# Kernel optimization log

Hardware: AMD Instinct MI355X
Metric: run time of the kernel (lower is better)

## Reference

```python
import jax, jax.numpy as jnp
import numpy as np

N = 50000      # nodes per type
E = 262144     # edges per relation
D_IN = 256; D_OUT = 256; D_ATT = 64
NEG_SLOPE = 0.2


def setup_inputs() -> dict:
    key = jax.random.key(0)
    ks = jax.random.split(key, 22)
    rn = lambda k, s, sc=0.05: jax.random.normal(k, s, jnp.float32) * sc
    ri = lambda k, s: jax.random.randint(k, s, 0, N, jnp.int32)
    return {
        "hA": jax.random.normal(ks[0], (N, D_IN), jnp.float32),
        "hB": jax.random.normal(ks[1], (N, D_IN), jnp.float32),
        "Wself": rn(ks[2], (2, D_IN, D_OUT)),
        "bself": rn(ks[3], (2, D_OUT), 0.01),
        "Wq": rn(ks[4], (2, D_OUT, D_ATT)),
        "bq": rn(ks[5], (2, D_ATT), 0.01),
        "Wk": rn(ks[6], (2, D_OUT, D_ATT)),
        "bk": rn(ks[7], (2, D_ATT), 0.01),
        "Wal": rn(ks[8], (2, D_ATT)),
        "bal": rn(ks[9], (2,), 0.01),
        "War": rn(ks[10], (2, D_ATT)),
        "bar": rn(ks[11], (2,), 0.01),
        "Wsrc": rn(ks[12], (2, D_IN, D_OUT)),
        "bsrc": rn(ks[13], (2, D_OUT), 0.01),
        "Wdst": rn(ks[14], (2, D_IN, D_OUT)),
        "bdst": rn(ks[15], (2, D_OUT), 0.01),
        "attn_v": rn(ks[16], (2, D_OUT)),
        "gbias": rn(ks[17], (2, D_OUT), 0.01),
        "eab_src": ri(ks[18], (E,)),
        "eab_dst": ri(ks[19], (E,)),
        "eba_src": ri(ks[20], (E,)),
        "eba_dst": ri(ks[21], (E,)),
    }


def _gatv2(h_src, h_dst, src, dst, Ws, bs, Wd, bd, av, gb, n_dst):
    """DGL GATv2Conv, num_heads=1: e_uv = av . leaky_relu(fc_src(h)[u] + fc_dst(h)[v]),
    edge-softmax over incoming edges per dst, message = alpha * fc_src(h)[u], + bias."""
    ft_s = h_src @ Ws + bs                              # (Ns, D)
    ft_d = h_dst @ Wd + bd                              # (Nd, D)
    e = jax.nn.leaky_relu(ft_s[src] + ft_d[dst], NEG_SLOPE)  # (E, D)
    logits = e @ av                                     # (E,)
    m = jax.ops.segment_max(logits, dst, num_segments=n_dst)
    m = jnp.where(jnp.isfinite(m), m, 0.0)              # zero-in-degree safety
    ex = jnp.exp(logits - m[dst])
    den = jax.ops.segment_sum(ex, dst, num_segments=n_dst)
    alpha = ex / jnp.where(den[dst] > 0, den[dst], 1.0)  # (E,) edge softmax
    out = jax.ops.segment_sum(alpha[:, None] * ft_s[src], dst, num_segments=n_dst) + gb
    return out, alpha


def _forward(hA, hB, Wself, bself, Wq, bq, Wk, bk, Wal, bal, War, bar,
             Wsrc, bsrc, Wdst, bdst, attn_v, gbias,
             eab_src, eab_dst, eba_src, eba_dst):
    h = [hA, hB]
    z = [h[t] @ Wself[t] + bself[t] for t in range(2)]       # HeteroLinear W_self
    q = [z[t] @ Wq[t] + bq[t] for t in range(2)]
    k = [z[t] @ Wk[t] + bk[t] for t in range(2)]
    h_l = [k[t] @ Wal[t] + bal[t] for t in range(2)]          # (N,) = W_al(key)
    h_r = [q[t] @ War[t] + bar[t] for t in range(2)]          # (N,) = W_ar(query)
    att_self = [jax.nn.elu(h_l[t] + h_r[t]) for t in range(2)]

    # relation "ab": A -> B (etype index 0)
    rst_ab, a_ab = _gatv2(hA, hB, eab_src, eab_dst,
                          Wsrc[0], bsrc[0], Wdst[0], bdst[0], attn_v[0], gbias[0], N)
    eatt_b = jax.nn.elu((rst_ab @ Wk[1] + bk[1]) @ Wal[1] + bal[1] + h_r[1])
    # relation "ba": B -> A (etype index 1)
    rst_ba, a_ba = _gatv2(hB, hA, eba_src, eba_dst,
                          Wsrc[1], bsrc[1], Wdst[1], bdst[1], attn_v[1], gbias[1], N)
    eatt_a = jax.nn.elu((rst_ba @ Wk[0] + bk[0]) @ Wal[0] + bal[0] + h_r[0])

    attA = jax.nn.softmax(jnp.stack([att_self[0], eatt_a]), axis=0)  # (2, N)
    attB = jax.nn.softmax(jnp.stack([att_self[1], eatt_b]), axis=0)
    rstA = jax.nn.elu(attA[0][:, None] * z[0] + attA[1][:, None] * rst_ba)
    rstB = jax.nn.elu(attB[0][:, None] * z[1] + attB[1][:, None] * rst_ab)
    return jnp.stack([rstA, rstB])  # (2, N, D_OUT)


def reference(hA, hB, Wself, bself, Wq, bq, Wk, bk, Wal, bal, War, bar,
              Wsrc, bsrc, Wdst, bdst, attn_v, gbias,
              eab_src, eab_dst, eba_src, eba_dst):
    return _forward(hA, hB, Wself, bself, Wq, bq, Wk, bk, Wal, bal, War, bar,
                    Wsrc, bsrc, Wdst, bdst, attn_v, gbias,
                    eab_src, eab_dst, eba_src, eba_dst)
```

## Files before the change

### kernel.cpp

```cpp
#include <hip/hip_runtime.h>
#include <math.h>

#define NNODES 50000
#define NEDGES 262144
#define NEG_SLOPE 0.2f
#define NBINS (2 * NNODES)
#define NXP 391
#define NWG_GEMM (2 * NXP * 6)

typedef __attribute__((ext_vector_type(8))) short short8;
typedef __attribute__((ext_vector_type(4))) float f32x4;
typedef __attribute__((ext_vector_type(2))) float f32x2;
typedef __attribute__((ext_vector_type(4))) unsigned short u16x4;

#define AUX_PS 0
#define AUX_PD (2 * NNODES)
#define AUX_HL (4 * NNODES)
#define AUX_HR (6 * NNODES)

__device__ __forceinline__ float elu_f(float x) { return x > 0.f ? x : (__expf(x) - 1.f); }
__device__ __forceinline__ float bf2f(unsigned short u) {
    return __uint_as_float(((unsigned)u) << 16);
}
__device__ __forceinline__ f32x2 bfp2f(unsigned p) {
    f32x2 r;
    r.x = __uint_as_float(p << 16);
    r.y = __uint_as_float(p & 0xffff0000u);
    return r;
}
__device__ __forceinline__ unsigned short f2bf(float f) {
    unsigned u = __float_as_uint(f);
    unsigned r = (u + 0x7fffu + ((u >> 16) & 1u)) >> 16;
    return (unsigned short)r;
}

__global__ __launch_bounds__(256) void conv_bf16_2(const float* __restrict__ inA,
                                                   const float* __restrict__ inB,
                                                   unsigned short* __restrict__ outA,
                                                   unsigned short* __restrict__ outB,
                                                   int half) {
    int i = (blockIdx.x * 256 + threadIdx.x) * 4;
    if (i >= 2 * half) return;
    const float* in = (i < half) ? inA : inB;
    unsigned short* out = (i < half) ? outA : outB;
    int k = (i < half) ? i : i - half;
    float4 v = *reinterpret_cast<const float4*>(&in[k]);
    u16x4 o;
    o[0] = f2bf(v.x); o[1] = f2bf(v.y); o[2] = f2bf(v.z); o[3] = f2bf(v.w);
    *reinterpret_cast<u16x4*>(&out[k]) = o;
}

__global__ __launch_bounds__(256) void prep_w(
    const float* __restrict__ Wself, const float* __restrict__ Wsrc, const float* __restrict__ Wdst,
    const float* __restrict__ bself, const float* __restrict__ bsrc, const float* __restrict__ bdst,
    unsigned short* __restrict__ Wt, float* __restrict__ biasF) {
    int r = blockIdx.x;
    int t = r / 768;
    int n = r % 768;
    int seg = n >> 8;
    int nn = n & 255;
    const float* W; const float* bv; int ti;
    if (seg == 0)      { W = Wself; bv = bself; ti = t; }
    else if (seg == 1) { W = Wsrc;  bv = bsrc;  ti = t; }
    else               { W = Wdst;  bv = bdst;  ti = 1 - t; }
    int k = threadIdx.x;
    float val = W[(size_t)ti * 65536 + (size_t)k * 256 + nn];
    Wt[(size_t)r * 256 + k] = f2bf(val);
    if (k == 0) biasF[r] = bv[ti * 256 + nn];
}

__global__ __launch_bounds__(256) void precompute_uv(
    const float* __restrict__ Wq, const float* __restrict__ bq,
    const float* __restrict__ Wk, const float* __restrict__ bk,
    const float* __restrict__ Wal, const float* __restrict__ bal,
    const float* __restrict__ War, const float* __restrict__ bar,
    float* __restrict__ u_l, float* __restrict__ u_r,
    float* __restrict__ c_l, float* __restrict__ c_r) {
    int t = blockIdx.x;
    int d = threadIdx.x;
    float sl = 0.f, sr = 0.f;
    for (int j = 0; j < 64; ++j) {
        sl += Wk[((size_t)t * 256 + d) * 64 + j] * Wal[t * 64 + j];
        sr += Wq[((size_t)t * 256 + d) * 64 + j] * War[t * 64 + j];
    }
    u_l[t * 256 + d] = sl;
    u_r[t * 256 + d] = sr;
    if (d == 0) {
        float cl = bal[t], cr = bar[t];
        for (int j = 0; j < 64; ++j) {
            cl += bk[t * 64 + j] * Wal[t * 64 + j];
            cr += bq[t * 64 + j] * War[t * 64 + j];
        }
        c_l[t] = cl; c_r[t] = cr;
    }
}

__global__ __launch_bounds__(256) void hist2(const int* __restrict__ dab,
                                             const int* __restrict__ dba,
                                             int* __restrict__ counts) {
    int e = blockIdx.x * 256 + threadIdx.x;
    if (e < NEDGES) atomicAdd(&counts[dab[e]], 1);
    else if (e < 2 * NEDGES) atomicAdd(&counts[NNODES + dba[e - NEDGES]], 1);
}

__global__ __launch_bounds__(256) void scan1(const int* __restrict__ counts,
                                             int* __restrict__ incl,
                                             int* __restrict__ bsum, int n) {
    __shared__ int s[256];
    int i = blockIdx.x * 256 + threadIdx.x;
    int t = threadIdx.x;
    s[t] = (i < n) ? counts[i] : 0;
    __syncthreads();
#pragma unroll
    for (int off = 1; off < 256; off <<= 1) {
        int x = (t >= off) ? s[t - off] : 0;
        __syncthreads();
        s[t] += x;
        __syncthreads();
    }
    if (i < n) incl[i] = s[t];
    if (t == 255) bsum[blockIdx.x] = s[255];
}

__global__ __launch_bounds__(512) void scan2(int* __restrict__ bsum, int nb) {
    __shared__ int s[512];
    int t = threadIdx.x;
    s[t] = (t < nb) ? bsum[t] : 0;
    __syncthreads();
#pragma unroll
    for (int off = 1; off < 512; off <<= 1) {
        int x = (t >= off) ? s[t - off] : 0;
        __syncthreads();
        s[t] += x;
        __syncthreads();
    }
    if (t < nb) bsum[t] = s[t];
}

__global__ __launch_bounds__(256) void scan3(const int* __restrict__ counts,
                                             int* __restrict__ incl_to_excl,
                                             const int* __restrict__ bsum,
                                             int* __restrict__ cursor, int n) {
    int i = blockIdx.x * 256 + threadIdx.x;
    if (i >= n) return;
    int base = (blockIdx.x > 0) ? bsum[blockIdx.x - 1] : 0;
    int st = base + incl_to_excl[i] - counts[i];
    incl_to_excl[i] = st;
    cursor[i] = st;
}

__global__ __launch_bounds__(256) void scatter2(const int* __restrict__ sab,
                                                const int* __restrict__ dab,
                                                const int* __restrict__ sba,
                                                const int* __restrict__ dba,
                                                int* __restrict__ cursor,
                                                int* __restrict__ sorted_src) {
    int e = blockIdx.x * 256 + threadIdx.x;
    if (e < NEDGES) {
        int pos = atomicAdd(&cursor[dab[e]], 1);
        sorted_src[pos] = sab[e];
    } else if (e < 2 * NEDGES) {
        int k = e - NEDGES;
        int pos = atomicAdd(&cursor[NNODES + dba[k]], 1);
        sorted_src[pos] = sba[k];
    }
}

__global__ __launch_bounds__(256) void gemm_mfma(
    const unsigned short* __restrict__ hAb,
    const unsigned short* __restrict__ hBb,
    const unsigned short* __restrict__ Wt,
    const float* __restrict__ biasF,
    const float* __restrict__ attn_v,
    const float* __restrict__ u_l,
    const float* __restrict__ u_r,
    unsigned short* __restrict__ bufA,
    unsigned short* __restrict__ bufB,
    float* __restrict__ aux,
    int M)
{
    __shared__ unsigned short lds[16384];
    const int tid = threadIdx.x;
    const int lane = tid & 63;
    const int w = tid >> 6;
    const int wm = w >> 1, wn = w & 1;

    const int nwg = NWG_GEMM;
    const int q = nwg / 8, r = nwg % 8;
    int orig = blockIdx.x;
    int xcd = orig % 8, idx = orig / 8;
    int wgid = (xcd < r) ? (xcd * (q + 1) + idx) : (r * (q + 1) + (xcd - r) * q + idx);
    int t   = wgid / (NXP * 6);
    int rem = wgid % (NXP * 6);
    int xp  = rem / 6;
    int yc  = rem % 6;

    const int row0 = xp * 128;
    const int col0 = yc * 128;
    const unsigned short* Ain = t ? hBb : hAb;
    const unsigned short* Wtt = Wt + (size_t)t * 768 * 256;
    const float* bias = biasF + t * 768;
    unsigned short* Cout = t ? bufB : bufA;

    f32x4 acc[4][4] = {};

    const unsigned short* gA[2];
    const unsigned short* gB[2];
#pragma unroll
    for (int rr = 0; rr < 2; ++rr) {
        int qq = rr * 256 + tid;
        int row = qq >> 2;
        int c = (qq & 3) ^ ((row >> 1) & 3);
        int ga = min(row0 + row, M - 1);
        gA[rr] = Ain + (size_t)ga * 256 + c * 8;
        gB[rr] = Wtt + (size_t)(col0 + row) * 256 + c * 8;
    }

#define STAGE(buf, kt)                                                                   \
    {                                                                                    \
        unsigned short* Ad = lds + (buf) * 4096;                                         \
        unsigned short* Bd = lds + 8192 + (buf) * 4096;                                  \
        _Pragma("unroll")                                                                \
        for (int rr = 0; rr < 2; ++rr) {                                                 \
            __builtin_amdgcn_global_load_lds(                                            \
                (const __attribute__((address_space(1))) unsigned int*)(gA[rr] + (kt)),  \
                (__attribute__((address_space(3))) unsigned int*)(Ad + ((rr * 256 + w * 64) << 3)), \
                16, 0, 0);                                                               \
            __builtin_amdgcn_global_load_lds(                                            \
                (const __attribute__((address_space(1))) unsigned int*)(gB[rr] + (kt)),  \
                (__attribute__((address_space(3))) unsigned int*)(Bd + ((rr * 256 + w * 64) << 3)), \
                16, 0, 0);                                                               \
        }                                                                                \
    }

    STAGE(0, 0);
    STAGE(1, 32);

#pragma unroll
    for (int it = 0; it < 8; ++it) {
        const int cur = it & 1;
        if (it < 7) { asm volatile("s_waitcnt vmcnt(4)" ::: "memory"); }
        else        { asm volatile("s_waitcnt vmcnt(0)" ::: "memory"); }
        __builtin_amdgcn_s_barrier();
        __builtin_amdgcn_sched_barrier(0);

        const unsigned short* As = lds + cur * 4096;
        const unsigned short* Bs = lds + 8192 + cur * 4096;
        short8 a[4], b[4];
#pragma unroll
        for (int i = 0; i < 4; ++i) {
            int ar = wm * 64 + i * 16 + (lane & 15);
            a[i] = *reinterpret_cast<const short8*>(
                &As[ar * 32 + (((lane >> 4) ^ ((ar >> 1) & 3)) << 3)]);
            int br = wn * 64 + i * 16 + (lane & 15);
            b[i] = *reinterpret_cast<const short8*>(
                &Bs[br * 32 + (((lane >> 4) ^ ((br >> 1) & 3)) << 3)]);
        }
#pragma unroll
        for (int i = 0; i < 4; ++i)
#pragma unroll
            for (int j = 0; j < 4; ++j)
                acc[i][j] = __builtin_amdgcn_mfma_f32_16x16x32_bf16(a[i], b[j], acc[i][j], 0, 0, 0);

        asm volatile("s_waitcnt lgkmcnt(0)" ::: "memory");
        __builtin_amdgcn_sched_barrier(0);
        __builtin_amdgcn_s_barrier();
        if (it < 6) STAGE(cur, (it + 2) * 32);
    }
#undef STAGE

#pragma unroll
    for (int j = 0; j < 4; ++j) {
        int colg = wn * 4 + j;
        int ci = lane & 15;
        float bv = bias[col0 + colg * 16 + ci];
#pragma unroll
        for (int i = 0; i < 4; ++i) {
            int rowb = wm * 64 + i * 16 + ((lane >> 4) << 2);
#pragma unroll
            for (int v = 0; v < 4; ++v) {
                int row = rowb + v;
                int g2 = colg ^ ((row >> 2) & 3);
                lds[row * 128 + g2 * 16 + ci] = f2bf(acc[i][j][v] + bv);
            }
        }
    }
    __syncthreads();

    const int seg = yc >> 1;
    const float* avp1; float* axp1;
    const float* avp2 = nullptr; float* axp2 = nullptr;
    if (seg == 0) {
        avp1 = u_l + t * 256;            axp1 = aux + AUX_HL + (size_t)t * NNODES;
        avp2 = u_r + t * 256;            axp2 = aux + AUX_HR + (size_t)t * NNODES;
    } else if (seg == 1) {
        avp1 = attn_v + t * 256;         axp1 = aux + AUX_PS + (size_t)t * NNODES;
    } else {
        avp1 = attn_v + (1 - t) * 256;   axp1 = aux + AUX_PD + (size_t)(1 - t) * NNODES;
    }

#pragma unroll
    for (int p = 0; p < 8; ++p) {
        int idx = p * 256 + tid;
        int row = idx >> 4;
        int ch = idx & 15;
        int g2 = (ch >> 1) ^ ((row >> 2) & 3);
        int grow = row0 + row;
        bool ok = grow < M;
        short8 val = *reinterpret_cast<const short8*>(&lds[row * 128 + g2 * 16 + ((ch & 1) << 3)]);
        if (ok)
            *reinterpret_cast<short8*>(&Cout[(size_t)grow * 768 + col0 + ch * 8]) = val;
        int colb = (yc & 1) * 128 + ch * 8;
        float4 w0v = *reinterpret_cast<const float4*>(&avp1[colb]);
        float4 w1v = *reinterpret_cast<const float4*>(&avp1[colb + 4]);
        float p1 = w0v.x * bf2f((unsigned short)val[0]) + w0v.y * bf2f((unsigned short)val[1])
                 + w0v.z * bf2f((unsigned short)val[2]) + w0v.w * bf2f((unsigned short)val[3])
                 + w1v.x * bf2f((unsigned short)val[4]) + w1v.y * bf2f((unsigned short)val[5])
                 + w1v.z * bf2f((unsigned short)val[6]) + w1v.w * bf2f((unsigned short)val[7]);
        p1 += __shfl_xor(p1, 1);
        p1 += __shfl_xor(p1, 2);
        p1 += __shfl_xor(p1, 4);
        p1 += __shfl_xor(p1, 8);
        if ((tid & 15) == 0 && ok) atomicAdd(&axp1[grow], p1);
        if (avp2) {
            float4 y0 = *reinterpret_cast<const float4*>(&avp2[colb]);
            float4 y1 = *reinterpret_cast<const float4*>(&avp2[colb + 4]);
            float p2 = y0.x * bf2f((unsigned short)val[0]) + y0.y * bf2f((unsigned short)val[1])
                     + y0.z * bf2f((unsigned short)val[2]) + y0.w * bf2f((unsigned short)val[3])
                     + y1.x * bf2f((unsigned short)val[4]) + y1.y * bf2f((unsigned short)val[5])
                     + y1.z * bf2f((unsigned short)val[6]) + y1.w * bf2f((unsigned short)val[7]);
            p2 += __shfl_xor(p2, 1);
            p2 += __shfl_xor(p2, 2);
            p2 += __shfl_xor(p2, 4);
            p2 += __shfl_xor(p2, 8);
            if ((tid & 15) == 0 && ok) atomicAdd(&axp2[grow], p2);
        }
    }
}

__global__ __launch_bounds__(256) void gat_fused(
    const unsigned short* __restrict__ bufA, const unsigned short* __restrict__ bufB,
    const int* __restrict__ sorted_src, const int* __restrict__ row_start,
    const int* __restrict__ counts,
    const float* __restrict__ attn_v, const float* __restrict__ gbias,
    const float* __restrict__ u_l,
    const float* __restrict__ c_l, const float* __restrict__ c_r,
    const float* __restrict__ aux,
    float* __restrict__ out)
{
    const int tid = threadIdx.x;
    const int l = tid & 15;
    const int gBase = tid & 48;
    const int nd = blockIdx.x * 16 + (tid >> 4);
    if (nd >= 2 * NNODES) return;
    const int rel = nd >= NNODES;
    const int d = nd - rel * NNODES;
    const int td = rel ? 0 : 1;

    const unsigned short* zbuf = td ? bufB : bufA;
    const unsigned short* ftS = (rel ? bufB : bufA) + 256;
    const unsigned short* ftD = zbuf + 512;
    const float clv = c_l[td], crv = c_r[td];

    f32x2 fd2[8], av2[8];
    {
        const unsigned short* fdp = &ftD[(size_t)d * 768 + l * 16];
        uint4 d0 = *reinterpret_cast<const uint4*>(fdp);
        uint4 d1 = *reinterpret_cast<const uint4*>(fdp + 8);
        fd2[0] = bfp2f(d0.x); fd2[1] = bfp2f(d0.y); fd2[2] = bfp2f(d0.z); fd2[3] = bfp2f(d0.w);
        fd2[4] = bfp2f(d1.x); fd2[5] = bfp2f(d1.y); fd2[6] = bfp2f(d1.z); fd2[7] = bfp2f(d1.w);
        const float* avp = attn_v + rel * 256 + l * 16;
#pragma unroll
        for (int e = 0; e < 4; ++e) {
            float4 a = *reinterpret_cast<const float4*>(&avp[e * 4]);
            av2[2 * e].x = a.x; av2[2 * e].y = a.y;
            av2[2 * e + 1].x = a.z; av2[2 * e + 1].y = a.w;
        }
    }

    const float pd6 = 0.6f * aux[AUX_PD + (size_t)rel * NNODES + d];
    const float hlv = aux[AUX_HL + (size_t)td * NNODES + d] + clv;
    const float hrv = aux[AUX_HR + (size_t)td * NNODES + d] + crv;
    const float a0 = elu_f(hlv + hrv);
    const float* psb = aux + AUX_PS + (size_t)rel * NNODES;

    const int p0  = row_start[nd];
    const int cnt = counts[nd];
    float den = 0.f;
    f32x2 acc2[8];
#pragma unroll
    for (int e = 0; e < 8; ++e) { acc2[e].x = 0.f; acc2[e].y = 0.f; }

    for (int base = 0; base < cnt; base += 16) {
        int nloc = min(16, cnt - base);
        int sv = 0; float psl = 0.f;
        if (base + l < cnt) { sv = sorted_src[p0 + base + l]; psl = psb[sv]; }
        int j = 0;
        for (; j + 2 <= nloc; j += 2) {
            int s0 = __shfl(sv, gBase + j);
            int s1 = __shfl(sv, gBase + j + 1);
            float q0 = __shfl(psl, gBase + j);
            float q1 = __shfl(psl, gBase + j + 1);
            const unsigned short* rp0 = &ftS[(size_t)s0 * 768 + l * 16];
            const unsigned short* rp1 = &ftS[(size_t)s1 * 768 + l * 16];
            uint4 A0 = *reinterpret_cast<const uint4*>(rp0);
            uint4 A1 = *reinterpret_cast<const uint4*>(rp0 + 8);
            uint4 B0 = *reinterpret_cast<const uint4*>(rp1);
            uint4 B1 = *reinterpret_cast<const uint4*>(rp1 + 8);
            f32x2 fa2[8], fb2[8];
            fa2[0] = bfp2f(A0.x); fa2[1] = bfp2f(A0.y); fa2[2] = bfp2f(A0.z); fa2[3] = bfp2f(A0.w);
            fa2[4] = bfp2f(A1.x); fa2[5] = bfp2f(A1.y); fa2[6] = bfp2f(A1.z); fa2[7] = bfp2f(A1.w);
            fb2[0] = bfp2f(B0.x); fb2[1] = bfp2f(B0.y); fb2[2] = bfp2f(B0.z); fb2[3] = bfp2f(B0.w);
            fb2[4] = bfp2f(B1.x); fb2[5] = bfp2f(B1.y); fb2[6] = bfp2f(B1.z); fb2[7] = bfp2f(B1.w);
            float Sa = 0.f, Sb = 0.f;
#pragma unroll
            for (int e = 0; e < 8; ++e) {
                f32x2 xa = fa2[e] + fd2[e];
                f32x2 xb = fb2[e] + fd2[e];
                Sa += av2[e].x * fabsf(xa.x);
                Sa += av2[e].y * fabsf(xa.y);
                Sb += av2[e].x * fabsf(xb.x);
                Sb += av2[e].y * fabsf(xb.y);
            }
            Sa += __shfl_xor(Sa, 1); Sb += __shfl_xor(Sb, 1);
            Sa += __shfl_xor(Sa, 2); Sb += __shfl_xor(Sb, 2);
            Sa += __shfl_xor(Sa, 4); Sb += __shfl_xor(Sb, 4);
            Sa += __shfl_xor(Sa, 8); Sb += __shfl_xor(Sb, 8);
            float wa = __expf(fmaf(0.6f, q0, pd6) + 0.4f * Sa);
            float wb = __expf(fmaf(0.6f, q1, pd6) + 0.4f * Sb);
            den += wa + wb;
#pragma unroll
            for (int e = 0; e < 8; ++e) acc2[e] += wa * fa2[e] + wb * fb2[e];
        }
        if (j < nloc) {
            int s0 = __shfl(sv, gBase + j);
            float q0 = __shfl(psl, gBase + j);
            const unsigned short* rp0 = &ftS[(size_t)s0 * 768 + l * 16];
            uint4 A0 = *reinterpret_cast<const uint4*>(rp0);
            uint4 A1 = *reinterpret_cast<const uint4*>(rp0 + 8);
            f32x2 fa2[8];
            fa2[0] = bfp2f(A0.x); fa2[1] = bfp2f(A0.y); fa2[2] = bfp2f(A0.z); fa2[3] = bfp2f(A0.w);
            fa2[4] = bfp2f(A1.x); fa2[5] = bfp2f(A1.y); fa2[6] = bfp2f(A1.z); fa2[7] = bfp2f(A1.w);
            float Sa = 0.f;
#pragma unroll
            for (int e = 0; e < 8; ++e) {
                f32x2 xa = fa2[e] + fd2[e];
                Sa += av2[e].x * fabsf(xa.x);
                Sa += av2[e].y * fabsf(xa.y);
            }
            Sa += __shfl_xor(Sa, 1);
            Sa += __shfl_xor(Sa, 2);
            Sa += __shfl_xor(Sa, 4);
            Sa += __shfl_xor(Sa, 8);
            float wa = __expf(fmaf(0.6f, q0, pd6) + 0.4f * Sa);
            den += wa;
#pragma unroll
            for (int e = 0; e < 8; ++e) acc2[e] += wa * fa2[e];
        }
    }

    float inv = den > 0.f ? 1.f / den : 1.f;
    const float* gb = gbias + rel * 256 + l * 16;
    const float* ulp = u_l + td * 256 + l * 16;
    f32x2 v2[8];
    float dotv = 0.f;
#pragma unroll
    for (int e = 0; e < 4; ++e) {
        float4 g = *reinterpret_cast<const float4*>(&gb[e * 4]);
        float4 u = *reinterpret_cast<const float4*>(&ulp[e * 4]);
        v2[2 * e].x     = acc2[2 * e].x     * inv + g.x;
        v2[2 * e].y     = acc2[2 * e].y     * inv + g.y;
        v2[2 * e + 1].x = acc2[2 * e + 1].x * inv + g.z;
        v2[2 * e + 1].y = acc2[2 * e + 1].y * inv + g.w;
        dotv += v2[2 * e].x * u.x + v2[2 * e].y * u.y
              + v2[2 * e + 1].x * u.z + v2[2 * e + 1].y * u.w;
    }
    dotv += __shfl_xor(dotv, 1);
    dotv += __shfl_xor(dotv, 2);
    dotv += __shfl_xor(dotv, 4);
    dotv += __shfl_xor(dotv, 8);
    const float ea = elu_f(dotv + clv + hrv);

    float mx = fmaxf(a0, ea);
    float e0 = __expf(a0 - mx), e1 = __expf(ea - mx);
    float is = 1.f / (e0 + e1);
    float w0 = e0 * is, w1 = e1 * is;

    const unsigned short* zrow = zbuf + (size_t)d * 768 + l * 16;
    uint4 z0 = *reinterpret_cast<const uint4*>(zrow);
    uint4 z1 = *reinterpret_cast<const uint4*>(zrow + 8);
    f32x2 zf2[8];
    zf2[0] = bfp2f(z0.x); zf2[1] = bfp2f(z0.y); zf2[2] = bfp2f(z0.z); zf2[3] = bfp2f(z0.w);
    zf2[4] = bfp2f(z1.x); zf2[5] = bfp2f(z1.y); zf2[6] = bfp2f(z1.z); zf2[7] = bfp2f(z1.w);

    float* orow = out + ((size_t)(1 - rel) * NNODES + d) * 256 + l * 16;
#pragma unroll
    for (int e = 0; e < 4; ++e) {
        float4 o;
        o.x = elu_f(w0 * zf2[2 * e].x     + w1 * v2[2 * e].x);
        o.y = elu_f(w0 * zf2[2 * e].y     + w1 * v2[2 * e].y);
        o.z = elu_f(w0 * zf2[2 * e + 1].x + w1 * v2[2 * e + 1].x);
        o.w = elu_f(w0 * zf2[2 * e + 1].y + w1 * v2[2 * e + 1].y);
        *reinterpret_cast<float4*>(&orow[e * 4]) = o;
    }
}

extern "C" void kernel_launch(void* const* d_in, const int* in_sizes, int n_in,
                              void* d_out, int out_size, void* d_ws, size_t ws_size,
                              hipStream_t stream) {
    const float* hA     = (const float*)d_in[0];
    const float* hB     = (const float*)d_in[1];
    const float* Wself  = (const float*)d_in[2];
    const float* bself  = (const float*)d_in[3];
    const float* Wq     = (const float*)d_in[4];
    const float* bq     = (const float*)d_in[5];
    const float* Wk     = (const float*)d_in[6];
    const float* bk     = (const float*)d_in[7];
    const float* Wal    = (const float*)d_in[8];
    const float* bal    = (const float*)d_in[9];
    const float* War    = (const float*)d_in[10];
    const float* bar    = (const float*)d_in[11];
    const float* Wsrc   = (const float*)d_in[12];
    const float* bsrc   = (const float*)d_in[13];
    const float* Wdst   = (const float*)d_in[14];
    const float* bdst   = (const float*)d_in[15];
    const float* attn_v = (const float*)d_in[16];
    const float* gbias  = (const float*)d_in[17];
    const int* eab_src  = (const int*)d_in[18];
    const int* eab_dst  = (const int*)d_in[19];
    const int* eba_src  = (const int*)d_in[20];
    const int* eba_dst  = (const int*)d_in[21];
    float* out = (float*)d_out;
    char* ws = (char*)d_ws;

    const size_t SZ_BUF = (size_t)NNODES * 768 * sizeof(unsigned short);
    const size_t SZ_H   = (size_t)NNODES * 256 * sizeof(unsigned short);
    size_t off = 0;
    auto alloc = [&](size_t bytes) { void* p = ws + off; off = (off + bytes + 255) & ~(size_t)255; return p; };
    unsigned short* bufA = (unsigned short*)alloc(SZ_BUF);
    unsigned short* bufB = (unsigned short*)alloc(SZ_BUF);
    unsigned short* hAb  = (unsigned short*)alloc(SZ_H);
    unsigned short* hBb  = (unsigned short*)alloc(SZ_H);
    unsigned short* Wt   = (unsigned short*)alloc(2 * 768 * 256 * sizeof(unsigned short));
    float* biasF   = (float*)alloc(2 * 768 * sizeof(float));
    float* aux     = (float*)alloc((size_t)8 * NNODES * sizeof(float));
    int* counts    = (int*)alloc(NBINS * sizeof(int));
    int* row_start = (int*)alloc(NBINS * sizeof(int));
    int* cursor    = (int*)alloc(NBINS * sizeof(int));
    int* bsum      = (int*)alloc(512 * sizeof(int));
    int* sorted_src= (int*)alloc(2 * (size_t)NEDGES * sizeof(int));
    float* u_l     = (float*)alloc(2 * 256 * sizeof(float));
    float* u_r     = (float*)alloc(2 * 256 * sizeof(float));
    float* c_l     = (float*)alloc(2 * sizeof(float));
    float* c_r     = (float*)alloc(2 * sizeof(float));

    hipMemsetAsync(counts, 0, NBINS * sizeof(int), stream);
    hipMemsetAsync(aux, 0, (size_t)8 * NNODES * sizeof(float), stream);
    precompute_uv<<<2, 256, 0, stream>>>(Wq, bq, Wk, bk, Wal, bal, War, bar, u_l, u_r, c_l, c_r);

    const int HN = NNODES * 256;
    conv_bf16_2<<<(2 * HN / 4 + 255) / 256, 256, 0, stream>>>(hA, hB, hAb, hBb, HN);
    prep_w<<<2 * 768, 256, 0, stream>>>(Wself, Wsrc, Wdst, bself, bsrc, bdst, Wt, biasF);

    const int e2blocks = (2 * NEDGES + 255) / 256;
    hist2<<<e2blocks, 256, 0, stream>>>(eab_dst, eba_dst, counts);
    const int sblocks = (NBINS + 255) / 256;
    scan1<<<sblocks, 256, 0, stream>>>(counts, row_start, bsum, NBINS);
    scan2<<<1, 512, 0, stream>>>(bsum, sblocks);
    scan3<<<sblocks, 256, 0, stream>>>(counts, row_start, bsum, cursor, NBINS);
    scatter2<<<e2blocks, 256, 0, stream>>>(eab_src, eab_dst, eba_src, eba_dst, cursor, sorted_src);

    gemm_mfma<<<NWG_GEMM, 256, 0, stream>>>(hAb, hBb, Wt, biasF, attn_v, u_l, u_r,
                                            bufA, bufB, aux, NNODES);

    gat_fused<<<(2 * NNODES + 15) / 16, 256, 0, stream>>>(bufA, bufB, sorted_src, row_start,
                                                          counts, attn_v, gbias, u_l,
                                                          c_l, c_r, aux, out);
}
```

Measured before the change: 272.6 us.

## Merge prep kernels, vectorize scans, unroll edge gather by four, bound GEMM occupancy

After: 272.6 us. About the same (-0.0%).

```diff
diff --git a/kernel.cpp b/kernel.cpp
--- a/kernel.cpp
+++ b/kernel.cpp
@@ -50,11 +50,37 @@
     *reinterpret_cast<u16x4*>(&out[k]) = o;
 }
 
-__global__ __launch_bounds__(256) void prep_w(
+__global__ __launch_bounds__(256) void prep_all(
     const float* __restrict__ Wself, const float* __restrict__ Wsrc, const float* __restrict__ Wdst,
     const float* __restrict__ bself, const float* __restrict__ bsrc, const float* __restrict__ bdst,
-    unsigned short* __restrict__ Wt, float* __restrict__ biasF) {
-    int r = blockIdx.x;
+    const float* __restrict__ Wq, const float* __restrict__ bq,
+    const float* __restrict__ Wk, const float* __restrict__ bk,
+    const float* __restrict__ Wal, const float* __restrict__ bal,
+    const float* __restrict__ War, const float* __restrict__ bar,
+    unsigned short* __restrict__ Wt, float* __restrict__ biasF,
+    float* __restrict__ u_l, float* __restrict__ u_r,
+    float* __restrict__ c_l, float* __restrict__ c_r) {
+    if (blockIdx.x < 2) {
+        int t = blockIdx.x;
+        int d = threadIdx.x;
+        float sl = 0.f, sr = 0.f;
+        for (int j = 0; j < 64; ++j) {
+            sl += Wk[((size_t)t * 256 + d) * 64 + j] * Wal[t * 64 + j];
+            sr += Wq[((size_t)t * 256 + d) * 64 + j] * War[t * 64 + j];
+        }
+        u_l[t * 256 + d] = sl;
+        u_r[t * 256 + d] = sr;
+        if (d == 0) {
+            float cl = bal[t], cr = bar[t];
+            for (int j = 0; j < 64; ++j) {
+                cl += bk[t * 64 + j] * Wal[t * 64 + j];
+                cr += bq[t * 64 + j] * War[t * 64 + j];
+            }
+            c_l[t] = cl; c_r[t] = cr;
+        }
+        return;
+    }
+    int r = blockIdx.x - 2;
     int t = r / 768;
     int n = r % 768;
     int seg = n >> 8;
@@ -69,32 +95,6 @@
     if (k == 0) biasF[r] = bv[ti * 256 + nn];
 }
 
-__global__ __launch_bounds__(256) void precompute_uv(
-    const float* __restrict__ Wq, const float* __restrict__ bq,
-    const float* __restrict__ Wk, const float* __restrict__ bk,
-    const float* __restrict__ Wal, const float* __restrict__ bal,
-    const float* __restrict__ War, const float* __restrict__ bar,
-    float* __restrict__ u_l, float* __restrict__ u_r,
-    float* __restrict__ c_l, float* __restrict__ c_r) {
-    int t = blockIdx.x;
-    int d = threadIdx.x;
-    float sl = 0.f, sr = 0.f;
-    for (int j = 0; j < 64; ++j) {
-        sl += Wk[((size_t)t * 256 + d) * 64 + j] * Wal[t * 64 + j];
-        sr += Wq[((size_t)t * 256 + d) * 64 + j] * War[t * 64 + j];
-    }
-    u_l[t * 256 + d] = sl;
-    u_r[t * 256 + d] = sr;
-    if (d == 0) {
-        float cl = bal[t], cr = bar[t];
-        for (int j = 0; j < 64; ++j) {
-            cl += bk[t * 64 + j] * Wal[t * 64 + j];
-            cr += bq[t * 64 + j] * War[t * 64 + j];
-        }
-        c_l[t] = cl; c_r[t] = cr;
-    }
-}
-
 __global__ __launch_bounds__(256) void hist2(const int* __restrict__ dab,
                                              const int* __restrict__ dba,
                                              int* __restrict__ counts) {
@@ -103,13 +103,16 @@
     else if (e < 2 * NEDGES) atomicAdd(&counts[NNODES + dba[e - NEDGES]], 1);
 }
 
-__global__ __launch_bounds__(256) void scan1(const int* __restrict__ counts,
-                                             int* __restrict__ incl,
-                                             int* __restrict__ bsum, int n) {
+__global__ __launch_bounds__(256) void scan1v(const int* __restrict__ counts,
+                                              int* __restrict__ incl,
+                                              int* __restrict__ bsum, int n) {
     __shared__ int s[256];
-    int i = blockIdx.x * 256 + threadIdx.x;
     int t = threadIdx.x;
-    s[t] = (i < n) ? counts[i] : 0;
+    int base = blockIdx.x * 1024 + t * 4;
+    int4 v = make_int4(0, 0, 0, 0);
+    if (base < n) v = *reinterpret_cast<const int4*>(&counts[base]);
+    int l0 = v.x, l1 = l0 + v.y, l2 = l1 + v.z, l3 = l2 + v.w;
+    s[t] = l3;
     __syncthreads();
 #pragma unroll
     for (int off = 1; off < 256; off <<= 1) {
@@ -118,7 +121,9 @@
         s[t] += x;
         __syncthreads();
     }
-    if (i < n) incl[i] = s[t];
+    int ex = s[t] - l3;
+    if (base < n)
+        *reinterpret_cast<int4*>(&incl[base]) = make_int4(ex + l0, ex + l1, ex + l2, ex + l3);
     if (t == 255) bsum[blockIdx.x] = s[255];
 }
 
@@ -137,16 +142,20 @@
     if (t < nb) bsum[t] = s[t];
 }
 
-__global__ __launch_bounds__(256) void scan3(const int* __restrict__ counts,
-                                             int* __restrict__ incl_to_excl,
-                                             const int* __restrict__ bsum,
-                                             int* __restrict__ cursor, int n) {
-    int i = blockIdx.x * 256 + threadIdx.x;
-    if (i >= n) return;
-    int base = (blockIdx.x > 0) ? bsum[blockIdx.x - 1] : 0;
-    int st = base + incl_to_excl[i] - counts[i];
-    incl_to_excl[i] = st;
-    cursor[i] = st;
+__global__ __launch_bounds__(256) void scan3v(const int* __restrict__ counts,
+                                              int* __restrict__ incl_to_rs,
+                                              const int* __restrict__ bsum,
+                                              int* __restrict__ cursor, int n, int nb) {
+    int base = blockIdx.x * 1024 + threadIdx.x * 4;
+    if (blockIdx.x == 0 && threadIdx.x == 0) incl_to_rs[n] = bsum[nb - 1];
+    if (base >= n) return;
+    int bofs = (blockIdx.x > 0) ? bsum[blockIdx.x - 1] : 0;
+    int4 ic = *reinterpret_cast<const int4*>(&incl_to_rs[base]);
+    int4 cn = *reinterpret_cast<const int4*>(&counts[base]);
+    int4 st = make_int4(bofs + ic.x - cn.x, bofs + ic.y - cn.y,
+                        bofs + ic.z - cn.z, bofs + ic.w - cn.w);
+    *reinterpret_cast<int4*>(&incl_to_rs[base]) = st;
+    *reinterpret_cast<int4*>(&cursor[base]) = st;
 }
 
 __global__ __launch_bounds__(256) void scatter2(const int* __restrict__ sab,
@@ -166,7 +175,7 @@
     }
 }
 
-__global__ __launch_bounds__(256) void gemm_mfma(
+__global__ __launch_bounds__(256, 4) void gemm_mfma(
     const unsigned short* __restrict__ hAb,
     const unsigned short* __restrict__ hBb,
     const unsigned short* __restrict__ Wt,
@@ -341,7 +350,6 @@
 __global__ __launch_bounds__(256) void gat_fused(
     const unsigned short* __restrict__ bufA, const unsigned short* __restrict__ bufB,
     const int* __restrict__ sorted_src, const int* __restrict__ row_start,
-    const int* __restrict__ counts,
     const float* __restrict__ attn_v, const float* __restrict__ gbias,
     const float* __restrict__ u_l,
     const float* __restrict__ c_l, const float* __restrict__ c_r,
@@ -385,17 +393,73 @@
     const float* psb = aux + AUX_PS + (size_t)rel * NNODES;
 
     const int p0  = row_start[nd];
-    const int cnt = counts[nd];
+    const int cnt = row_start[nd + 1] - p0;
     float den = 0.f;
     f32x2 acc2[8];
 #pragma unroll
     for (int e = 0; e < 8; ++e) { acc2[e].x = 0.f; acc2[e].y = 0.f; }
+
+#define PROC2(X0, X1, QX, Y0, Y1, QY)                                            \
+    {                                                                            \
+        f32x2 fa2[8], fb2[8];                                                    \
+        fa2[0] = bfp2f((X0).x); fa2[1] = bfp2f((X0).y);                          \
+        fa2[2] = bfp2f((X0).z); fa2[3] = bfp2f((X0).w);                          \
+        fa2[4] = bfp2f((X1).x); fa2[5] = bfp2f((X1).y);                          \
+        fa2[6] = bfp2f((X1).z); fa2[7] = bfp2f((X1).w);                          \
+        fb2[0] = bfp2f((Y0).x); fb2[1] = bfp2f((Y0).y);                          \
+        fb2[2] = bfp2f((Y0).z); fb2[3] = bfp2f((Y0).w);                          \
+        fb2[4] = bfp2f((Y1).x); fb2[5] = bfp2f((Y1).y);                          \
+        fb2[6] = bfp2f((Y1).z); fb2[7] = bfp2f((Y1).w);                          \
+        float Sa = 0.f, Sb = 0.f;                                                \
+        _Pragma("unroll")                                                        \
+        for (int e = 0; e < 8; ++e) {                                            \
+            f32x2 xa = fa2[e] + fd2[e];                                          \
+            f32x2 xb = fb2[e] + fd2[e];                                          \
+            Sa += av2[e].x * fabsf(xa.x);                                        \
+            Sa += av2[e].y * fabsf(xa.y);                                        \
+            Sb += av2[e].x * fabsf(xb.x);                                        \
+            Sb += av2[e].y * fabsf(xb.y);                                        \
+        }                                                                        \
+        Sa += __shfl_xor(Sa, 1); Sb += __shfl_xor(Sb, 1);                        \
+        Sa += __shfl_xor(Sa, 2); Sb += __shfl_xor(Sb, 2);                        \
+        Sa += __shfl_xor(Sa, 4); Sb += __shfl_xor(Sb, 4);                        \
+        Sa += __shfl_xor(Sa, 8); Sb += __shfl_xor(Sb, 8);                        \
+        float wa = __expf(fmaf(0.6f, (QX), pd6) + 0.4f * Sa);                    \
+        float wb = __expf(fmaf(0.6f, (QY), pd6) + 0.4f * Sb);                    \
+        den += wa + wb;                                                          \
+        _Pragma("unroll")                                                        \
+        for (int e = 0; e < 8; ++e) acc2[e] += wa * fa2[e] + wb * fb2[e];        \
+    }
 
     for (int base = 0; base < cnt; base += 16) {
         int nloc = min(16, cnt - base);
         int sv = 0; float psl = 0.f;
         if (base + l < cnt) { sv = sorted_src[p0 + base + l]; psl = psb[sv]; }
         int j = 0;
+        for (; j + 4 <= nloc; j += 4) {
+            int s0 = __shfl(sv, gBase + j);
+            int s1 = __shfl(sv, gBase + j + 1);
+            int s2 = __shfl(sv, gBase + j + 2);
+            int s3 = __shfl(sv, gBase + j + 3);
+            float q0 = __shfl(psl, gBase + j);
+            float q1 = __shfl(psl, gBase + j + 1);
+            float q2 = __shfl(psl, gBase + j + 2);
+            float q3 = __shfl(psl, gBase + j + 3);
+            const unsigned short* rp0 = &ftS[(size_t)s0 * 768 + l * 16];
+            const unsigned short* rp1 = &ftS[(size_t)s1 * 768 + l * 16];
+            const unsigned short* rp2 = &ftS[(size_t)s2 * 768 + l * 16];
+            const unsigned short* rp3 = &ftS[(size_t)s3 * 768 + l * 16];
+            uint4 A0 = *reinterpret_cast<const uint4*>(rp0);
+            uint4 A1 = *reinterpret_cast<const uint4*>(rp0 + 8);
+            uint4 B0 = *reinterpret_cast<const uint4*>(rp1);
+            uint4 B1 = *reinterpret_cast<const uint4*>(rp1 + 8);
+            uint4 C0 = *reinterpret_cast<const uint4*>(rp2);
+            uint4 C1 = *reinterpret_cast<const uint4*>(rp2 + 8);
+            uint4 D0 = *reinterpret_cast<const uint4*>(rp3);
+            uint4 D1 = *reinterpret_cast<const uint4*>(rp3 + 8);
+            PROC2(A0, A1, q0, B0, B1, q1);
+            PROC2(C0, C1, q2, D0, D1, q3);
+        }
         for (; j + 2 <= nloc; j += 2) {
             int s0 = __shfl(sv, gBase + j);
             int s1 = __shfl(sv, gBase + j + 1);
@@ -407,30 +471,7 @@
             uint4 A1 = *reinterpret_cast<const uint4*>(rp0 + 8);
             uint4 B0 = *reinterpret_cast<const uint4*>(rp1);
             uint4 B1 = *reinterpret_cast<const uint4*>(rp1 + 8);
-            f32x2 fa2[8], fb2[8];
-            fa2[0] = bfp2f(A0.x); fa2[1] = bfp2f(A0.y); fa2[2] = bfp2f(A0.z); fa2[3] = bfp2f(A0.w);
-            fa2[4] = bfp2f(A1.x); fa2[5] = bfp2f(A1.y); fa2[6] = bfp2f(A1.z); fa2[7] = bfp2f(A1.w);
-            fb2[0] = bfp2f(B0.x); fb2[1] = bfp2f(B0.y); fb2[2] = bfp2f(B0.z); fb2[3] = bfp2f(B0.w);
-            fb2[4] = bfp2f(B1.x); fb2[5] = bfp2f(B1.y); fb2[6] = bfp2f(B1.z); fb2[7] = bfp2f(B1.w);
-            float Sa = 0.f, Sb = 0.f;
-#pragma unroll
-            for (int e = 0; e < 8; ++e) {
-                f32x2 xa = fa2[e] + fd2[e];
-                f32x2 xb = fb2[e] + fd2[e];
-                Sa += av2[e].x * fabsf(xa.x);
-                Sa += av2[e].y * fabsf(xa.y);
-                Sb += av2[e].x * fabsf(xb.x);
-                Sb += av2[e].y * fabsf(xb.y);
-            }
-            Sa += __shfl_xor(Sa, 1); Sb += __shfl_xor(Sb, 1);
-            Sa += __shfl_xor(Sa, 2); Sb += __shfl_xor(Sb, 2);
-            Sa += __shfl_xor(Sa, 4); Sb += __shfl_xor(Sb, 4);
-            Sa += __shfl_xor(Sa, 8); Sb += __shfl_xor(Sb, 8);
-            float wa = __expf(fmaf(0.6f, q0, pd6) + 0.4f * Sa);
-            float wb = __expf(fmaf(0.6f, q1, pd6) + 0.4f * Sb);
-            den += wa + wb;
-#pragma unroll
-            for (int e = 0; e < 8; ++e) acc2[e] += wa * fa2[e] + wb * fb2[e];
+            PROC2(A0, A1, q0, B0, B1, q1);
         }
         if (j < nloc) {
             int s0 = __shfl(sv, gBase + j);
@@ -458,6 +499,7 @@
             for (int e = 0; e < 8; ++e) acc2[e] += wa * fa2[e];
         }
     }
+#undef PROC2
 
     float inv = den > 0.f ? 1.f / den : 1.f;
     const float* gb = gbias + rel * 256 + l * 16;
@@ -545,7 +587,7 @@
     float* biasF   = (float*)alloc(2 * 768 * sizeof(float));
     float* aux     = (float*)alloc((size_t)8 * NNODES * sizeof(float));
     int* counts    = (int*)alloc(NBINS * sizeof(int));
-    int* row_start = (int*)alloc(NBINS * sizeof(int));
+    int* row_start = (int*)alloc((NBINS + 4) * sizeof(int));
     int* cursor    = (int*)alloc(NBINS * sizeof(int));
     int* bsum      = (int*)alloc(512 * sizeof(int));
     int* sorted_src= (int*)alloc(2 * (size_t)NEDGES * sizeof(int));
@@ -556,24 +598,25 @@
 
     hipMemsetAsync(counts, 0, NBINS * sizeof(int), stream);
     hipMemsetAsync(aux, 0, (size_t)8 * NNODES * sizeof(float), stream);
-    precompute_uv<<<2, 256, 0, stream>>>(Wq, bq, Wk, bk, Wal, bal, War, bar, u_l, u_r, c_l, c_r);
 
     const int HN = NNODES * 256;
     conv_bf16_2<<<(2 * HN / 4 + 255) / 256, 256, 0, stream>>>(hA, hB, hAb, hBb, HN);
-    prep_w<<<2 * 768, 256, 0, stream>>>(Wself, Wsrc, Wdst, bself, bsrc, bdst, Wt, biasF);
+    prep_all<<<2 + 2 * 768, 256, 0, stream>>>(Wself, Wsrc, Wdst, bself, bsrc, bdst,
+                                              Wq, bq, Wk, bk, Wal, bal, War, bar,
+                                              Wt, biasF, u_l, u_r, c_l, c_r);
 
     const int e2blocks = (2 * NEDGES + 255) / 256;
     hist2<<<e2blocks, 256, 0, stream>>>(eab_dst, eba_dst, counts);
-    const int sblocks = (NBINS + 255) / 256;
-    scan1<<<sblocks, 256, 0, stream>>>(counts, row_start, bsum, NBINS);
+    const int sblocks = (NBINS + 1023) / 1024;
+    scan1v<<<sblocks, 256, 0, stream>>>(counts, row_start, bsum, NBINS);
     scan2<<<1, 512, 0, stream>>>(bsum, sblocks);
-    scan3<<<sblocks, 256, 0, stream>>>(counts, row_start, bsum, cursor, NBINS);
+    scan3v<<<sblocks, 256, 0, stream>>>(counts, row_start, bsum, cursor, NBINS, sblocks);
     scatter2<<<e2blocks, 256, 0, stream>>>(eab_src, eab_dst, eba_src, eba_dst, cursor, sorted_src);
 
     gemm_mfma<<<NWG_GEMM, 256, 0, stream>>>(hAb, hBb, Wt, biasF, attn_v, u_l, u_r,
                                             bufA, bufB, aux, NNODES);
 
     gat_fused<<<(2 * NNODES + 15) / 16, 256, 0, stream>>>(bufA, bufB, sorted_src, row_start,
-                                                          counts, attn_v, gbias, u_l,
+                                                          attn_v, gbias, u_l,
                                                           c_l, c_r, aux, out);
 }
```
